# Kernel optimization log

Hardware: AMD Instinct MI355X
Metric: run time of the kernel (lower is better)

Reference implementation:

```python
import jax, jax.numpy as jnp
import numpy as np

HIDDEN = 4096
NUM_HEADS = 32
NUM_KV_HEADS = 8
HEAD_DIM = 128
EPS = 1e-6
ROPE_THETA = 1000000.0
T = 2048


def setup_inputs() -> dict:
    key = jax.random.key(0)
    k1, k2, k3, k4, k5 = jax.random.split(key, 5)
    q_size = NUM_HEADS * HEAD_DIM
    kv_size = NUM_KV_HEADS * HEAD_DIM
    return {
        "positions": jnp.arange(T, dtype=jnp.int32),
        "hidden_states": jax.random.normal(k1, (T, HIDDEN), dtype=jnp.float32),
        "w_qkv": jax.random.normal(k2, (HIDDEN, q_size + 2 * kv_size), dtype=jnp.float32) * 0.02,
        "w_o": jax.random.normal(k3, (q_size, HIDDEN), dtype=jnp.float32) * 0.02,
        "q_norm_w": jnp.ones((HEAD_DIM,), dtype=jnp.float32) + 0.01 * jax.random.normal(k4, (HEAD_DIM,), dtype=jnp.float32),
        "k_norm_w": jnp.ones((HEAD_DIM,), dtype=jnp.float32) + 0.01 * jax.random.normal(k5, (HEAD_DIM,), dtype=jnp.float32),
    }


def _rms_norm(x, w, eps=EPS):
    # x: [..., head_dim], normalize over last dim
    var = jnp.mean(jnp.square(x), axis=-1, keepdims=True)
    return x * jax.lax.rsqrt(var + eps) * w


def _apply_rope(x, positions):
    # neox-style rotate-half RoPE, rotary_dim == head_dim
    d = x.shape[-1]
    inv_freq = 1.0 / (ROPE_THETA ** (jnp.arange(0, d, 2, dtype=jnp.float32) / d))
    freqs = positions.astype(jnp.float32)[:, None] * inv_freq[None, :]  # [T, d/2]
    cos = jnp.cos(freqs)[:, None, :]  # [T, 1, d/2]
    sin = jnp.sin(freqs)[:, None, :]
    x1, x2 = jnp.split(x, 2, axis=-1)
    return jnp.concatenate([x1 * cos - x2 * sin, x2 * cos + x1 * sin], axis=-1)


def reference(positions, hidden_states, w_qkv, w_o, q_norm_w, k_norm_w):
    num_tokens = hidden_states.shape[0]
    q_size = NUM_HEADS * HEAD_DIM
    kv_size = NUM_KV_HEADS * HEAD_DIM
    group = NUM_HEADS // NUM_KV_HEADS

    qkv = hidden_states @ w_qkv  # [T, q+2kv]
    q = qkv[:, :q_size].reshape(num_tokens, NUM_HEADS, HEAD_DIM)
    k = qkv[:, q_size:q_size + kv_size].reshape(num_tokens, NUM_KV_HEADS, HEAD_DIM)
    v = qkv[:, q_size + kv_size:].reshape(num_tokens, NUM_KV_HEADS, HEAD_DIM)

    q = _rms_norm(q, q_norm_w)
    k = _rms_norm(k, k_norm_w)
    q = _apply_rope(q, positions)
    k = _apply_rope(k, positions)

    scale = HEAD_DIM ** -0.5
    # GQA: group query heads over shared kv heads
    qg = q.reshape(num_tokens, NUM_KV_HEADS, group, HEAD_DIM)
    scores = jnp.einsum("tkgd,skd->kgts", qg * scale, k)  # [KH, G, T, S]
    causal = positions[:, None] >= positions[None, :]  # [T, S]
    scores = jnp.where(causal[None, None, :, :], scores, jnp.finfo(scores.dtype).min)
    probs = jax.nn.softmax(scores, axis=-1)
    out = jnp.einsum("kgts,skd->tkgd", probs, v)  # [T, KH, G, D]
    out = out.reshape(num_tokens, q_size)
    return out @ w_o
```

## Files before the change

### kernel.cpp

```cpp
#include <hip/hip_runtime.h>
#include <cstdint>
#include <cstddef>

#define T_TOK 2048
#define HID   4096
#define NQH   32
#define NKVH  8
#define HD    128
#define QKV_N 6144

typedef __bf16 bf16x8 __attribute__((ext_vector_type(8)));
typedef __bf16 bf16x4 __attribute__((ext_vector_type(4)));
typedef float  f32x4  __attribute__((ext_vector_type(4)));
typedef float  f32x16 __attribute__((ext_vector_type(16)));

#define AS1 __attribute__((address_space(1)))
#define AS3 __attribute__((address_space(3)))

__device__ __forceinline__ void gll16(const void* g, void* l) {
  __builtin_amdgcn_global_load_lds((const AS1 void*)g, (AS3 void*)l, 16, 0, 0);
}

__global__ __launch_bounds__(256) void k_convert(const float* __restrict__ in,
                                                 __bf16* __restrict__ out, int n4) {
  int i = blockIdx.x * 256 + threadIdx.x;
  if (i >= n4) return;
  float4 v = ((const float4*)in)[i];
  bf16x4 o;
  o[0] = (__bf16)v.x; o[1] = (__bf16)v.y; o[2] = (__bf16)v.z; o[3] = (__bf16)v.w;
  ((bf16x4*)out)[i] = o;
}

__global__ __launch_bounds__(256) void k_transpose(const float* __restrict__ in,
                                                   __bf16* __restrict__ out,
                                                   int R, int C) {
  __shared__ float tile[32][33];
  int c0 = blockIdx.x * 32, r0 = blockIdx.y * 32;
  int tx = threadIdx.x, ty = threadIdx.y;
#pragma unroll
  for (int k = 0; k < 4; ++k)
    tile[ty + k*8][tx] = in[(size_t)(r0 + ty + k*8) * C + c0 + tx];
  __syncthreads();
#pragma unroll
  for (int k = 0; k < 4; ++k)
    out[(size_t)(c0 + ty + k*8) * R + r0 + tx] = (__bf16)tile[tx][ty + k*8];
}

template <int NFR>
__global__ __launch_bounds__(512, 2) void k_gemm2p(const __bf16* __restrict__ A,
                                                   const __bf16* __restrict__ Bt,
                                                   float* __restrict__ C,
                                                   int N, int K) {
  constexpr int BN   = 64 * NFR;
  constexpr int WN   = 16 * NFR;
  constexpr int NB   = NFR / 2;
  constexpr int BREG = BN * 64;
  constexpr int BUFSZ = 16384 + 2 * BREG;
  __shared__ alignas(16) char ldsb[2 * BUFSZ];
  const int tid = threadIdx.x;
  const int lane = tid & 63, w = tid >> 6;
  const int l16 = lane & 15, lg = lane >> 4;
  const int wm = w >> 2, wn = w & 3;

  const int x = blockIdx.x & 7, idx = blockIdx.x >> 3;
  const int bm = (x & 1) * 8 + (idx & 7);
  const int bn = (x >> 1) * 4 + (idx >> 3);

  const int rA = tid >> 2, pA = tid & 3;
  const __bf16* asrc = A + (size_t)(bm * 128 + rA) * K + ((pA ^ ((rA >> 1) & 3)) * 8);
  const __bf16* bsrc = Bt + (size_t)(bn * BN + rA) * K + ((pA ^ ((rA >> 1) & 3)) * 8);

#define RA_(buf, mk) (ldsb + (buf) * BUFSZ + (mk) * 8192)
#define RB_(buf, mk) (ldsb + (buf) * BUFSZ + 16384 + (mk) * BREG)
#define STG_A(buf, mk, kk) { gll16(asrc + (kk) + (mk) * 32, RA_(buf, mk) + w * 1024); }
#define STG_B(buf, mk, kk) { _Pragma("unroll") \
    for (int j = 0; j < NB; ++j) \
      gll16(bsrc + (size_t)j * 128 * K + (kk) + (mk) * 32, RB_(buf, mk) + j * 8192 + w * 1024); }
#define FRAG(base, row) (*(const bf16x8*)((base) + (row) * 64 + ((lg ^ (((row) >> 1) & 3)) << 4)))
#define WAITN() { if constexpr (NFR == 6) asm volatile("s_waitcnt vmcnt(8)" ::: "memory"); \
                  else                    asm volatile("s_waitcnt vmcnt(6)" ::: "memory"); }

  f32x4 acc[4][NFR] = {};
  const int nkt = K >> 6;

  STG_A(0, 0, 0); STG_B(0, 0, 0); STG_A(0, 1, 0); STG_B(0, 1, 0);

  for (int t = 0; t < nkt - 1; ++t) {
    const int cur = t & 1, nxt = cur ^ 1;
    const int kn = (t + 1) * 64;
    bf16x8 af[4], bf_[NFR];

    STG_A(nxt, 0, kn); STG_B(nxt, 0, kn);
    WAITN();
    __builtin_amdgcn_s_barrier();
    __builtin_amdgcn_sched_barrier(0);
#pragma unroll
    for (int i = 0; i < 4; ++i) af[i] = FRAG(RA_(cur, 0), wm * 64 + i * 16 + l16);
#pragma unroll
    for (int n = 0; n < NFR; ++n) bf_[n] = FRAG(RB_(cur, 0), wn * WN + n * 16 + l16);
    __builtin_amdgcn_s_setprio(1);
#pragma unroll
    for (int i = 0; i < 4; ++i)
#pragma unroll
      for (int n = 0; n < NFR; ++n)
        acc[i][n] = __builtin_amdgcn_mfma_f32_16x16x32_bf16(af[i], bf_[n], acc[i][n], 0, 0, 0);
    __builtin_amdgcn_s_setprio(0);

    STG_A(nxt, 1, kn); STG_B(nxt, 1, kn);
    WAITN();
    __builtin_amdgcn_s_barrier();
    __builtin_amdgcn_sched_barrier(0);
#pragma unroll
    for (int i = 0; i < 4; ++i) af[i] = FRAG(RA_(cur, 1), wm * 64 + i * 16 + l16);
#pragma unroll
    for (int n = 0; n < NFR; ++n) bf_[n] = FRAG(RB_(cur, 1), wn * WN + n * 16 + l16);
    __builtin_amdgcn_s_setprio(1);
#pragma unroll
    for (int i = 0; i < 4; ++i)
#pragma unroll
      for (int n = 0; n < NFR; ++n)
        acc[i][n] = __builtin_amdgcn_mfma_f32_16x16x32_bf16(af[i], bf_[n], acc[i][n], 0, 0, 0);
    __builtin_amdgcn_s_setprio(0);
    __builtin_amdgcn_s_barrier();
  }

  asm volatile("s_waitcnt vmcnt(0)" ::: "memory");
  __builtin_amdgcn_s_barrier();
  __builtin_amdgcn_sched_barrier(0);
  {
    const int cur = (nkt - 1) & 1;
#pragma unroll
    for (int mk = 0; mk < 2; ++mk) {
      bf16x8 aa[4], bb[NFR];
#pragma unroll
      for (int i = 0; i < 4; ++i) aa[i] = FRAG(RA_(cur, mk), wm * 64 + i * 16 + l16);
#pragma unroll
      for (int n = 0; n < NFR; ++n) bb[n] = FRAG(RB_(cur, mk), wn * WN + n * 16 + l16);
#pragma unroll
      for (int i = 0; i < 4; ++i)
#pragma unroll
        for (int n = 0; n < NFR; ++n)
          acc[i][n] = __builtin_amdgcn_mfma_f32_16x16x32_bf16(aa[i], bb[n], acc[i][n], 0, 0, 0);
    }
  }
#undef RA_
#undef RB_
#undef STG_A
#undef STG_B
#undef FRAG
#undef WAITN

#pragma unroll
  for (int mi = 0; mi < 4; ++mi)
#pragma unroll
    for (int ni = 0; ni < NFR; ++ni) {
      int row = bm * 128 + wm * 64 + mi * 16 + lg * 4;
      int col = bn * BN + wn * WN + ni * 16 + l16;
#pragma unroll
      for (int r = 0; r < 4; ++r)
        C[(size_t)(row + r) * N + col] = acc[mi][ni][r];
    }
}

__global__ __launch_bounds__(64) void k_norm_rope(const float* __restrict__ qkv,
                                                  const int* __restrict__ pos,
                                                  const float* __restrict__ qw,
                                                  const float* __restrict__ kw,
                                                  __bf16* __restrict__ qo,
                                                  __bf16* __restrict__ ko,
                                                  __bf16* __restrict__ vto) {
  const int slot = blockIdx.x;
  const int t    = blockIdx.y;
  const int i    = threadIdx.x;
  const int off  = (slot < 32) ? slot * 128
                 : (slot < 40) ? 4096 + (slot - 32) * 128
                                : 5120 + (slot - 40) * 128;
  const float* base = qkv + (size_t)t * QKV_N + off;
  float x1 = base[i], x2 = base[i + 64];
  if (slot >= 40) {
    __bf16* o = vto + ((size_t)(slot - 40) * HD) * T_TOK + t;
    o[(size_t)i * T_TOK] = (__bf16)x1;
    o[(size_t)(i + 64) * T_TOK] = (__bf16)x2;
    return;
  }
  float ss = x1 * x1 + x2 * x2;
#pragma unroll
  for (int m = 32; m >= 1; m >>= 1) ss += __shfl_xor(ss, m);
  float rinv = rsqrtf(ss * (1.0f / 128.0f) + 1e-6f);
  const float* wn = (slot < 32) ? qw : kw;
  float n1 = x1 * rinv * wn[i];
  float n2 = x2 * rinv * wn[i + 64];
  float fr = (float)pos[t] * expf((float)i * -0.21586735246819178f);
  float cs = cosf(fr), sn = sinf(fr);
  float o1 = n1 * cs - n2 * sn;
  float o2 = n2 * cs + n1 * sn;
  if (slot < 32) {
    const float QSC = 0.08838834764831845f * 1.4426950408889634f;
    __bf16* o = qo + ((size_t)t * NQH + slot) * HD;
    o[i] = (__bf16)(o1 * QSC);
    o[i + 64] = (__bf16)(o2 * QSC);
  } else {
    __bf16* o = ko + ((size_t)t * NKVH + (slot - 32)) * HD;
    o[i] = (__bf16)o1;
    o[i + 64] = (__bf16)o2;
  }
}

__global__ __launch_bounds__(256, 2) void k_attn(const __bf16* __restrict__ Q,
                                                 const __bf16* __restrict__ K,
                                                 const __bf16* __restrict__ Vt,
                                                 __bf16* __restrict__ O) {
  __shared__ alignas(16) __bf16 Ks[64 * 128];
  __shared__ alignas(16) __bf16 Vts[128 * 64];
  const int bid = blockIdx.x;
  const int kvh = bid & 7;
  const int qc  = bid >> 3;
  const int tid = threadIdx.x, lane = tid & 63, w = tid >> 6;
  const int l31 = lane & 31, hi = lane >> 5;
  const int h  = kvh * 4 + w;
  const int q0 = qc * 32;
  const int qrow = q0 + l31;
  char* Ksb = (char*)Ks;
  char* Vtb = (char*)Vts;

  bf16x8 qf[8];
  {
    const __bf16* qp = Q + ((size_t)qrow * NQH + h) * HD + hi * 8;
#pragma unroll
    for (int dc = 0; dc < 8; ++dc)
      qf[dc] = *(const bf16x8*)(qp + dc * 16);
  }

  size_t ksrc[4], vsrc[4];
#pragma unroll
  for (int j = 0; j < 4; ++j) {
    int kr = w * 16 + j * 4 + (lane >> 4);
    ksrc[j] = ((size_t)kr * NKVH + kvh) * HD + (size_t)(((lane & 15) ^ (kr & 15)) * 8);
    int vr = w * 32 + j * 8 + (lane >> 3);
    vsrc[j] = ((size_t)(kvh * HD + vr)) * T_TOK + (size_t)(((lane & 7) ^ (vr & 7)) * 8);
  }

  float m_run = -3.0e38f, l_run = 0.f;
  f32x16 ot[4] = {};

  const int ntiles = (qc >> 1) + 1;
  for (int tt = 0; tt < ntiles; ++tt) {
    const int s0 = tt * 64;
#pragma unroll
    for (int j = 0; j < 4; ++j) {
      gll16(K + (size_t)s0 * (NKVH * HD) + ksrc[j], Ksb + (w * 4 + j) * 1024);
      gll16(Vt + (size_t)s0 + vsrc[j], Vtb + (w * 4 + j) * 1024);
    }
    __syncthreads();

    f32x16 sac[2] = {};
#pragma unroll
    for (int hf = 0; hf < 2; ++hf) {
      int krow = hf * 32 + l31;
#pragma unroll
      for (int dc = 0; dc < 8; ++dc) {
        bf16x8 kf = *(const bf16x8*)(Ksb + krow * 256 + (((dc * 2 + hi) ^ (krow & 15)) * 16));
        sac[hf] = __builtin_amdgcn_mfma_f32_32x32x16_bf16(kf, qf[dc], sac[hf], 0, 0, 0);
      }
    }

    float pv[32];
    if (s0 + 64 > q0) {
#pragma unroll
      for (int hf = 0; hf < 2; ++hf)
#pragma unroll
        for (int r = 0; r < 16; ++r) {
          int kvg = s0 + hf * 32 + (r & 3) + ((r >> 2) * 8) + hi * 4;
          pv[hf * 16 + r] = (kvg > qrow) ? -3.0e38f : sac[hf][r];
        }
    } else {
#pragma unroll
      for (int hf = 0; hf < 2; ++hf)
#pragma unroll
        for (int r = 0; r < 16; ++r) pv[hf * 16 + r] = sac[hf][r];
    }
    float t16[16];
#pragma unroll
    for (int i = 0; i < 16; ++i) t16[i] = fmaxf(pv[i], pv[i + 16]);
#pragma unroll
    for (int i = 0; i < 8; ++i) t16[i] = fmaxf(t16[i], t16[i + 8]);
#pragma unroll
    for (int i = 0; i < 4; ++i) t16[i] = fmaxf(t16[i], t16[i + 4]);
    float mt = fmaxf(fmaxf(t16[0], t16[1]), fmaxf(t16[2], t16[3]));
    mt = fmaxf(mt, __shfl_xor(mt, 32));
    if (!__all(mt - m_run <= 10.0f)) {
      float m_new = fmaxf(m_run, mt);
      float corr = exp2f(m_run - m_new);
      l_run *= corr;
#pragma unroll
      for (int dt = 0; dt < 4; ++dt)
#pragma unroll
        for (int r = 0; r < 16; ++r) ot[dt][r] *= corr;
      m_run = m_new;
    }
#pragma unroll
    for (int i = 0; i < 32; ++i) pv[i] = exp2f(pv[i] - m_run);
#pragma unroll
    for (int i = 0; i < 16; ++i) t16[i] = pv[i] + pv[i + 16];
#pragma unroll
    for (int i = 0; i < 8; ++i) t16[i] += t16[i + 8];
#pragma unroll
    for (int i = 0; i < 4; ++i) t16[i] += t16[i + 4];
    float rs = (t16[0] + t16[1]) + (t16[2] + t16[3]);
    rs += __shfl_xor(rs, 32);
    l_run += rs;

    uint32_t wds[16];
#pragma unroll
    for (int i = 0; i < 16; ++i) {
      uint32_t r;
      asm("v_cvt_pk_bf16_f32 %0, %1, %2" : "=v"(r) : "v"(pv[2 * i]), "v"(pv[2 * i + 1]));
      wds[i] = r;
    }
#pragma unroll
    for (int c = 0; c < 4; ++c) {
      const int base = (c >> 1) * 8 + (c & 1) * 4;
      uint32_t sa = hi ? wds[base + 0] : wds[base + 2];
      uint32_t sb = hi ? wds[base + 1] : wds[base + 3];
      uint32_t ra = __shfl_xor(sa, 32);
      uint32_t rb = __shfl_xor(sb, 32);
      union { uint32_t u[4]; bf16x8 v; } pf;
      pf.u[0] = hi ? ra : wds[base + 0];
      pf.u[1] = hi ? rb : wds[base + 1];
      pf.u[2] = hi ? wds[base + 2] : ra;
      pf.u[3] = hi ? wds[base + 3] : rb;
#pragma unroll
      for (int dt = 0; dt < 4; ++dt) {
        int vrow = dt * 32 + l31;
        bf16x8 vf = *(const bf16x8*)(Vtb + vrow * 128 + (((c * 2 + hi) ^ (vrow & 7)) * 16));
        ot[dt] = __builtin_amdgcn_mfma_f32_32x32x16_bf16(vf, pf.v, ot[dt], 0, 0, 0);
      }
    }
    __syncthreads();
  }

  float inv = 1.0f / l_run;
  char* Ob = Ksb + w * 8192;
#pragma unroll
  for (int dt = 0; dt < 4; ++dt)
#pragma unroll
    for (int r = 0; r < 16; ++r) {
      int d = dt * 32 + (r & 3) + ((r >> 2) * 8) + hi * 4;
      *(__bf16*)(Ob + l31 * 256 + ((d * 2) ^ ((l31 & 7) << 4))) = (__bf16)(ot[dt][r] * inv);
    }
#pragma unroll
  for (int pass = 0; pass < 8; ++pass) {
    int q = pass * 4 + (lane >> 4);
    int ch = lane & 15;
    bf16x8 vvv = *(const bf16x8*)(Ob + q * 256 + ((ch ^ (q & 7)) * 16));
    *(bf16x8*)(O + ((size_t)(q0 + q) * NQH + h) * HD + ch * 8) = vvv;
  }
}

extern "C" void kernel_launch(void* const* d_in, const int* in_sizes, int n_in,
                              void* d_out, int out_size, void* d_ws, size_t ws_size,
                              hipStream_t stream) {
  const int*   positions = (const int*)d_in[0];
  const float* hidden    = (const float*)d_in[1];
  const float* w_qkv     = (const float*)d_in[2];
  const float* w_o       = (const float*)d_in[3];
  const float* q_norm    = (const float*)d_in[4];
  const float* k_norm    = (const float*)d_in[5];
  float* out = (float*)d_out;

  char* ws = (char*)d_ws;
  __bf16* wqkv_t   = (__bf16*)ws;
  __bf16* wo_t     = (__bf16*)(ws + 50331648);
  __bf16* hidden_b = (__bf16*)(ws + 83886080);
  float*  qkv      = (float*)(ws + 100663296);
  __bf16* qb  = (__bf16*)ws;
  __bf16* kb  = (__bf16*)(ws + 16777216);
  __bf16* vtb = (__bf16*)(ws + 20971520);
  __bf16* attn_o = hidden_b;

  k_convert<<<dim3((T_TOK * HID / 4 + 255) / 256), 256, 0, stream>>>(hidden, hidden_b, T_TOK * HID / 4);
  k_transpose<<<dim3(QKV_N / 32, HID / 32), dim3(32, 8), 0, stream>>>(w_qkv, wqkv_t, HID, QKV_N);
  k_transpose<<<dim3(HID / 32, HID / 32), dim3(32, 8), 0, stream>>>(w_o, wo_t, HID, HID);
  k_gemm2p<6><<<dim3(256), 512, 0, stream>>>(hidden_b, wqkv_t, qkv, QKV_N, HID);
  k_norm_rope<<<dim3(48, T_TOK), 64, 0, stream>>>(qkv, positions, q_norm, k_norm, qb, kb, vtb);
  k_attn<<<dim3(512), 256, 0, stream>>>(qb, kb, vtb, attn_o);
  k_gemm2p<4><<<dim3(256), 512, 0, stream>>>(attn_o, wo_t, out, HID, HID);
}
```

Before: 328.6 us.

## Switch GEMMs to 32x32x16 MFMA and merge the two K-half stages per iteration

Replaces the 16x16x32 bf16 MFMA tiling with 32x32x16 MFMA fragments, so each wave computes its tile with fewer, larger instructions and fewer LDS fragment reads per FLOP. It also issues both half-tile prefetches up front and does a single wait and barrier per 64-wide K step instead of two. The intent is to raise MFMA efficiency and cut synchronisation overhead in both projection GEMMs. In exchange, the larger accumulators raise register pressure and the output store pattern becomes more strided, and the single barrier reduces overlap between loads and compute.

```diff
diff --git a/kernel.cpp b/kernel.cpp
--- a/kernel.cpp
+++ b/kernel.cpp
@@ -46,20 +46,19 @@
     out[(size_t)(c0 + ty + k*8) * R + r0 + tx] = (__bf16)tile[tx][ty + k*8];
 }
 
-template <int NFR>
-__global__ __launch_bounds__(512, 2) void k_gemm2p(const __bf16* __restrict__ A,
+template <int NF32>
+__global__ __launch_bounds__(512, 2) void k_gemm1w(const __bf16* __restrict__ A,
                                                    const __bf16* __restrict__ Bt,
                                                    float* __restrict__ C,
                                                    int N, int K) {
-  constexpr int BN   = 64 * NFR;
-  constexpr int WN   = 16 * NFR;
-  constexpr int NB   = NFR / 2;
+  constexpr int BN   = 128 * NF32;
+  constexpr int WN   = 32 * NF32;
   constexpr int BREG = BN * 64;
   constexpr int BUFSZ = 16384 + 2 * BREG;
   __shared__ alignas(16) char ldsb[2 * BUFSZ];
   const int tid = threadIdx.x;
   const int lane = tid & 63, w = tid >> 6;
-  const int l16 = lane & 15, lg = lane >> 4;
+  const int l31 = lane & 31, hi = lane >> 5;
   const int wm = w >> 2, wn = w & 3;
 
   const int x = blockIdx.x & 7, idx = blockIdx.x >> 3;
@@ -74,13 +73,13 @@
 #define RB_(buf, mk) (ldsb + (buf) * BUFSZ + 16384 + (mk) * BREG)
 #define STG_A(buf, mk, kk) { gll16(asrc + (kk) + (mk) * 32, RA_(buf, mk) + w * 1024); }
 #define STG_B(buf, mk, kk) { _Pragma("unroll") \
-    for (int j = 0; j < NB; ++j) \
+    for (int j = 0; j < NF32; ++j) \
       gll16(bsrc + (size_t)j * 128 * K + (kk) + (mk) * 32, RB_(buf, mk) + j * 8192 + w * 1024); }
-#define FRAG(base, row) (*(const bf16x8*)((base) + (row) * 64 + ((lg ^ (((row) >> 1) & 3)) << 4)))
-#define WAITN() { if constexpr (NFR == 6) asm volatile("s_waitcnt vmcnt(8)" ::: "memory"); \
-                  else                    asm volatile("s_waitcnt vmcnt(6)" ::: "memory"); }
-
-  f32x4 acc[4][NFR] = {};
+#define FRAG32(base, row, c) (*(const bf16x8*)((base) + (size_t)(row) * 64 + ((((c) ^ (((row) >> 1) & 3))) << 4)))
+#define WAITN() { if constexpr (NF32 == 3) asm volatile("s_waitcnt vmcnt(8)" ::: "memory"); \
+                  else                     asm volatile("s_waitcnt vmcnt(6)" ::: "memory"); }
+
+  f32x16 acc[2][NF32] = {};
   const int nkt = K >> 6;
 
   STG_A(0, 0, 0); STG_B(0, 0, 0); STG_A(0, 1, 0); STG_B(0, 1, 0);
@@ -88,39 +87,32 @@
   for (int t = 0; t < nkt - 1; ++t) {
     const int cur = t & 1, nxt = cur ^ 1;
     const int kn = (t + 1) * 64;
-    bf16x8 af[4], bf_[NFR];
 
     STG_A(nxt, 0, kn); STG_B(nxt, 0, kn);
-    WAITN();
-    __builtin_amdgcn_s_barrier();
-    __builtin_amdgcn_sched_barrier(0);
-#pragma unroll
-    for (int i = 0; i < 4; ++i) af[i] = FRAG(RA_(cur, 0), wm * 64 + i * 16 + l16);
-#pragma unroll
-    for (int n = 0; n < NFR; ++n) bf_[n] = FRAG(RB_(cur, 0), wn * WN + n * 16 + l16);
-    __builtin_amdgcn_s_setprio(1);
-#pragma unroll
-    for (int i = 0; i < 4; ++i)
-#pragma unroll
-      for (int n = 0; n < NFR; ++n)
-        acc[i][n] = __builtin_amdgcn_mfma_f32_16x16x32_bf16(af[i], bf_[n], acc[i][n], 0, 0, 0);
-    __builtin_amdgcn_s_setprio(0);
-
     STG_A(nxt, 1, kn); STG_B(nxt, 1, kn);
     WAITN();
     __builtin_amdgcn_s_barrier();
     __builtin_amdgcn_sched_barrier(0);
-#pragma unroll
-    for (int i = 0; i < 4; ++i) af[i] = FRAG(RA_(cur, 1), wm * 64 + i * 16 + l16);
-#pragma unroll
-    for (int n = 0; n < NFR; ++n) bf_[n] = FRAG(RB_(cur, 1), wn * WN + n * 16 + l16);
+
     __builtin_amdgcn_s_setprio(1);
 #pragma unroll
-    for (int i = 0; i < 4; ++i)
-#pragma unroll
-      for (int n = 0; n < NFR; ++n)
-        acc[i][n] = __builtin_amdgcn_mfma_f32_16x16x32_bf16(af[i], bf_[n], acc[i][n], 0, 0, 0);
+    for (int s = 0; s < 4; ++s) {
+      const int mk = s >> 1, c0 = (s & 1) * 2 + hi;
+      bf16x8 af[2], bfr[NF32];
+#pragma unroll
+      for (int mi = 0; mi < 2; ++mi)
+        af[mi] = FRAG32(RA_(cur, mk), wm * 64 + mi * 32 + l31, c0);
+#pragma unroll
+      for (int ni = 0; ni < NF32; ++ni)
+        bfr[ni] = FRAG32(RB_(cur, mk), wn * WN + ni * 32 + l31, c0);
+#pragma unroll
+      for (int mi = 0; mi < 2; ++mi)
+#pragma unroll
+        for (int ni = 0; ni < NF32; ++ni)
+          acc[mi][ni] = __builtin_amdgcn_mfma_f32_32x32x16_bf16(af[mi], bfr[ni], acc[mi][ni], 0, 0, 0);
+    }
     __builtin_amdgcn_s_setprio(0);
+    __builtin_amdgcn_sched_barrier(0);
     __builtin_amdgcn_s_barrier();
   }
 
@@ -130,35 +122,39 @@
   {
     const int cur = (nkt - 1) & 1;
 #pragma unroll
-    for (int mk = 0; mk < 2; ++mk) {
-      bf16x8 aa[4], bb[NFR];
-#pragma unroll
-      for (int i = 0; i < 4; ++i) aa[i] = FRAG(RA_(cur, mk), wm * 64 + i * 16 + l16);
-#pragma unroll
-      for (int n = 0; n < NFR; ++n) bb[n] = FRAG(RB_(cur, mk), wn * WN + n * 16 + l16);
-#pragma unroll
-      for (int i = 0; i < 4; ++i)
-#pragma unroll
-        for (int n = 0; n < NFR; ++n)
-          acc[i][n] = __builtin_amdgcn_mfma_f32_16x16x32_bf16(aa[i], bb[n], acc[i][n], 0, 0, 0);
+    for (int s = 0; s < 4; ++s) {
+      const int mk = s >> 1, c0 = (s & 1) * 2 + hi;
+      bf16x8 af[2], bfr[NF32];
+#pragma unroll
+      for (int mi = 0; mi < 2; ++mi)
+        af[mi] = FRAG32(RA_(cur, mk), wm * 64 + mi * 32 + l31, c0);
+#pragma unroll
+      for (int ni = 0; ni < NF32; ++ni)
+        bfr[ni] = FRAG32(RB_(cur, mk), wn * WN + ni * 32 + l31, c0);
+#pragma unroll
+      for (int mi = 0; mi < 2; ++mi)
+#pragma unroll
+        for (int ni = 0; ni < NF32; ++ni)
+          acc[mi][ni] = __builtin_amdgcn_mfma_f32_32x32x16_bf16(af[mi], bfr[ni], acc[mi][ni], 0, 0, 0);
     }
   }
 #undef RA_
 #undef RB_
 #undef STG_A
 #undef STG_B
-#undef FRAG
+#undef FRAG32
 #undef WAITN
 
 #pragma unroll
-  for (int mi = 0; mi < 4; ++mi)
-#pragma unroll
-    for (int ni = 0; ni < NFR; ++ni) {
-      int row = bm * 128 + wm * 64 + mi * 16 + lg * 4;
-      int col = bn * BN + wn * WN + ni * 16 + l16;
-#pragma unroll
-      for (int r = 0; r < 4; ++r)
-        C[(size_t)(row + r) * N + col] = acc[mi][ni][r];
+  for (int mi = 0; mi < 2; ++mi)
+#pragma unroll
+    for (int ni = 0; ni < NF32; ++ni) {
+      int colg = bn * BN + wn * WN + ni * 32 + l31;
+#pragma unroll
+      for (int r = 0; r < 16; ++r) {
+        int rowg = bm * 128 + wm * 64 + mi * 32 + (r & 3) + 8 * (r >> 2) + 4 * hi;
+        C[(size_t)rowg * N + colg] = acc[mi][ni][r];
+      }
     }
 }
 
@@ -381,8 +377,8 @@
   k_convert<<<dim3((T_TOK * HID / 4 + 255) / 256), 256, 0, stream>>>(hidden, hidden_b, T_TOK * HID / 4);
   k_transpose<<<dim3(QKV_N / 32, HID / 32), dim3(32, 8), 0, stream>>>(w_qkv, wqkv_t, HID, QKV_N);
   k_transpose<<<dim3(HID / 32, HID / 32), dim3(32, 8), 0, stream>>>(w_o, wo_t, HID, HID);
-  k_gemm2p<6><<<dim3(256), 512, 0, stream>>>(hidden_b, wqkv_t, qkv, QKV_N, HID);
+  k_gemm1w<3><<<dim3(256), 512, 0, stream>>>(hidden_b, wqkv_t, qkv, QKV_N, HID);
   k_norm_rope<<<dim3(48, T_TOK), 64, 0, stream>>>(qkv, positions, q_norm, k_norm, qb, kb, vtb);
   k_attn<<<dim3(512), 256, 0, stream>>>(qb, kb, vtb, attn_o);
-  k_gemm2p<4><<<dim3(256), 512, 0, stream>>>(attn_o, wo_t, out, HID, HID);
-}
+  k_gemm1w<2><<<dim3(256), 512, 0, stream>>>(attn_o, wo_t, out, HID, HID);
+}
```

New measurement: 361.8 us. +10.1%, slower.
